# Kernel tuning notes

Measured on AMD Instinct MI355X. Metric: run time of the kernel, lower is better.

Reference implementation:

```python
import jax, jax.numpy as jnp
import numpy as np

B, N, D, L = 8, 2048, 1024, 128


def setup_inputs() -> dict:
    key = jax.random.key(0)
    ks = jax.random.split(key, 8)
    return {
        "e_i_t_minus_1": jax.random.normal(ks[0], (B, D), dtype=jnp.float32),
        "e_j_t": jax.random.normal(ks[1], (B, N, D), dtype=jnp.float32),
        "imp_j_t": jax.random.uniform(ks[2], (B, N), dtype=jnp.float32),
        "R_lk": jax.random.normal(ks[3], (L, D), dtype=jnp.float32),
        "W_q": jax.random.normal(ks[4], (D, D), dtype=jnp.float32) * (D ** -0.5),
        "W_k": jax.random.normal(ks[5], (D, D), dtype=jnp.float32) * (D ** -0.5),
        "W_v": jax.random.normal(ks[6], (D, D), dtype=jnp.float32) * (D ** -0.5),
        "omega": jax.random.normal(ks[7], (D,), dtype=jnp.float32),
    }


def reference(e_i_t_minus_1, e_j_t, imp_j_t, R_lk, W_q, W_k, W_v, omega):
    # torch nn.Linear(x) = x @ W.T  (weights stored [out, in])
    q_i = jnp.einsum('bd,ed->be', e_i_t_minus_1, W_q)[:, None, :]   # [B,1,D]
    k_j = jnp.einsum('bnd,ed->bne', e_j_t, W_k)                      # [B,N,D]
    sigma = jnp.einsum('bnd,d->bn', jnp.tanh(q_i + k_j), omega)      # [B,N]
    exp_sigma = jnp.exp(sigma)
    sum_exp = jnp.sum(exp_sigma, axis=1, keepdims=True)              # [B,1]
    a_ij = imp_j_t * exp_sigma / (sum_exp + 1e-9)                    # [B,N]
    v_j = jnp.einsum('bnd,ed->bne', e_j_t, W_v)                      # [B,N,D]
    A = jnp.einsum('bn,bnd->bd', a_ij, v_j)                          # [B,D]
    # R_lk[l,d] * a_ij[b,n] * v_j[b,n,d], summed over n -> [B,L,D]
    A_lk = jnp.einsum('bn,bnd,ld->bld', a_ij, v_j, R_lk)             # [B,L,D]
    A_l = A                                                          # identical math in source
    return (A, A_lk, A_l)
```

## Files before the change

### kernel.cpp

```cpp
#include <hip/hip_runtime.h>
#include <hip/hip_bf16.h>
#include <math.h>

#define BB 8
#define NN 2048
#define DD 1024
#define LL 128
#define MM (BB*NN)

typedef _Float16 half8 __attribute__((ext_vector_type(8)));
typedef _Float16 half4 __attribute__((ext_vector_type(4)));
typedef __attribute__((ext_vector_type(4))) float floatx4;

__device__ __forceinline__ void glds16(const void* g, void* l) {
    __builtin_amdgcn_global_load_lds(
        (const __attribute__((address_space(1))) unsigned int*)g,
        (__attribute__((address_space(3))) unsigned int*)l, 16, 0, 0);
}

__device__ __forceinline__ float ftanh(float x) {
    float e = __expf(2.0f * x);
    return 1.0f - 2.0f * __builtin_amdgcn_rcpf(e + 1.0f);
}

__global__ __launch_bounds__(256) void prep_kernel(const float* __restrict__ e_j,
                                                   _Float16* __restrict__ eh,
                                                   const float* __restrict__ Wk,
                                                   _Float16* __restrict__ wh,
                                                   const float* __restrict__ e_i,
                                                   const float* __restrict__ Wq,
                                                   float* __restrict__ q) {
    __shared__ float us[BB][DD];
    int blk = blockIdx.x;
    int tid = threadIdx.x;
    if (blk < 8192) {
        int i = blk * 256 + tid;
        const float4* xp = (const float4*)e_j + (size_t)i * 2;
        float4 v0 = xp[0], v1 = xp[1];
        half8 h;
        h[0] = (_Float16)v0.x; h[1] = (_Float16)v0.y;
        h[2] = (_Float16)v0.z; h[3] = (_Float16)v0.w;
        h[4] = (_Float16)v1.x; h[5] = (_Float16)v1.y;
        h[6] = (_Float16)v1.z; h[7] = (_Float16)v1.w;
        *(half8*)(eh + (size_t)i * 8) = h;
    } else if (blk < 8704) {
        int i = (blk - 8192) * 256 + tid;
        const float4* xp = (const float4*)Wk + (size_t)i * 2;
        float4 v0 = xp[0], v1 = xp[1];
        half8 h;
        h[0] = (_Float16)v0.x; h[1] = (_Float16)v0.y;
        h[2] = (_Float16)v0.z; h[3] = (_Float16)v0.w;
        h[4] = (_Float16)v1.x; h[5] = (_Float16)v1.y;
        h[6] = (_Float16)v1.z; h[7] = (_Float16)v1.w;
        *(half8*)(wh + (size_t)i * 8) = h;
    } else {
        for (int i = tid; i < BB * DD / 4; i += 256)
            ((float4*)&us[0][0])[i] = ((const float4*)e_i)[i];
        __syncthreads();
        int w = tid >> 6, lane = tid & 63;
        int d = (blk - 8704) * 4 + w;
        float acc[8] = {0.f, 0.f, 0.f, 0.f, 0.f, 0.f, 0.f, 0.f};
        for (int e0 = 0; e0 < DD; e0 += 256) {
            float4 wv = *(const float4*)&Wq[(size_t)d * DD + e0 + lane * 4];
            #pragma unroll
            for (int r = 0; r < 8; ++r) {
                float4 uv = *(const float4*)&us[r][e0 + lane * 4];
                acc[r] += wv.x * uv.x + wv.y * uv.y + wv.z * uv.z + wv.w * uv.w;
            }
        }
        #pragma unroll
        for (int r = 0; r < 8; ++r) {
            float s = acc[r];
            #pragma unroll
            for (int off = 32; off; off >>= 1) s += __shfl_down(s, off, 64);
            if (lane == 0) q[r * DD + d] = s;
        }
    }
}

__global__ __launch_bounds__(512, 2) void sigma256(const _Float16* __restrict__ eh,
                                                   const _Float16* __restrict__ wh,
                                                   const float* __restrict__ q,
                                                   const float* __restrict__ omega,
                                                   float* __restrict__ sig_part)
{
    __shared__ _Float16 As[4][256][32];
    __shared__ _Float16 Bs[4][256][32];

    const int tid  = threadIdx.x;
    const int lane = tid & 63;
    const int wid  = tid >> 6;
    const int wr   = wid >> 2;
    const int wc   = wid & 3;
    const int c15  = lane & 15, quad = lane >> 4;

    const int wgid   = (blockIdx.x & 7) * 32 + (blockIdx.x >> 3);
    const int colBlk = wgid >> 6;
    const int rowBlk = wgid & 63;
    const int row0   = rowBlk * 256;
    const int col0   = colBlk * 256;
    const int b      = row0 / NN;

    const int srow = wid * 16 + (lane >> 2);
    const int ssub = ((lane & 3) ^ ((lane >> 3) & 3)) * 8;
    const _Float16* gA = eh + (size_t)(row0 + srow) * DD + ssub;
    const _Float16* gB = wh + (size_t)(col0 + srow) * DD + ssub;
    char* const ldsA0 = (char*)&As[0][0][0] + wid * 1024;
    char* const ldsB0 = (char*)&Bs[0][0][0] + wid * 1024;

#define STAGE_A(kt) do { int _bi = (kt) & 3; int _k0 = (kt) * 32;                  \
        glds16(gA + _k0,                    ldsA0 + _bi * 16384);                  \
        glds16(gA + (size_t)128 * DD + _k0, ldsA0 + _bi * 16384 + 8192); } while (0)
#define STAGE_B(kt) do { int _bi = (kt) & 3; int _k0 = (kt) * 32;                  \
        glds16(gB + _k0,                    ldsB0 + _bi * 16384);                  \
        glds16(gB + (size_t)128 * DD + _k0, ldsB0 + _bi * 16384 + 8192); } while (0)

    const char* const Abase = (const char*)&As[0][0][0];
    const char* const Bbase = (const char*)&Bs[0][0][0];
#define FRAG(base, bi, row, qd) \
    (*(const half8*)((base) + (bi) * 16384 + (row) * 64 + ((((qd) ^ (((row) >> 1) & 3))) << 4)))

    floatx4 acc[8][4];
    #pragma unroll
    for (int m = 0; m < 8; ++m)
        #pragma unroll
        for (int n = 0; n < 4; ++n) acc[m][n] = (floatx4){0.f, 0.f, 0.f, 0.f};

    half8 a03[4], a47[4], bb[4], bbn[4];

    STAGE_A(0); STAGE_B(0);
    STAGE_A(1); STAGE_B(1);
    STAGE_A(2); STAGE_B(2);
    asm volatile("s_waitcnt vmcnt(8)" ::: "memory");
    __builtin_amdgcn_s_barrier();
    __builtin_amdgcn_sched_barrier(0);
    #pragma unroll
    for (int n = 0; n < 4; ++n) bb[n]  = FRAG(Bbase, 0, wc * 64  + n * 16 + c15, quad);
    #pragma unroll
    for (int m = 0; m < 4; ++m) a03[m] = FRAG(Abase, 0, wr * 128 + m * 16 + c15, quad);

#define PH1(t_, DO_STAGE)                                                          \
    {                                                                              \
        const int bi = (t_) & 3;                                                   \
        _Pragma("unroll")                                                          \
        for (int m = 0; m < 4; ++m)                                                \
            a47[m] = FRAG(Abase, bi, wr * 128 + 64 + m * 16 + c15, quad);          \
        if (DO_STAGE) STAGE_A((t_) + 3);                                           \
        __builtin_amdgcn_sched_barrier(0);                                         \
        __builtin_amdgcn_s_setprio(1);                                             \
        _Pragma("unroll")                                                          \
        for (int m = 0; m < 4; ++m)                                                \
            _Pragma("unroll")                                                      \
            for (int n = 0; n < 4; ++n)                                            \
                acc[m][n] = __builtin_amdgcn_mfma_f32_16x16x32_f16(a03[m], bb[n], acc[m][n], 0, 0, 0); \
        __builtin_amdgcn_s_setprio(0);                                             \
    }

#define PH2(t_, DO_STAGE, DO_READS, VMW)                                           \
    {                                                                              \
        const int bin = ((t_) + 1) & 3;                                            \
        asm volatile("s_waitcnt vmcnt(" #VMW ")" ::: "memory");                    \
        asm volatile("s_waitcnt lgkmcnt(0)" ::: "memory");                         \
        __builtin_amdgcn_s_barrier();                                              \
        __builtin_amdgcn_sched_barrier(0);                                         \
        if (DO_READS) {                                                            \
            _Pragma("unroll")                                                      \
            for (int n = 0; n < 4; ++n)                                            \
                bbn[n] = FRAG(Bbase, bin, wc * 64  + n * 16 + c15, quad);          \
            _Pragma("unroll")                                                      \
            for (int m = 0; m < 4; ++m)                                            \
                a03[m] = FRAG(Abase, bin, wr * 128 + m * 16 + c15, quad);          \
        }                                                                          \
        if (DO_STAGE) STAGE_B((t_) + 3);                                           \
        __builtin_amdgcn_sched_barrier(0);                                         \
        __builtin_amdgcn_s_setprio(1);                                             \
        _Pragma("unroll")                                                          \
        for (int m = 0; m < 4; ++m)                                                \
            _Pragma("unroll")                                                      \
            for (int n = 0; n < 4; ++n)                                            \
                acc[4 + m][n] = __builtin_amdgcn_mfma_f32_16x16x32_f16(a47[m], bb[n], acc[4 + m][n], 0, 0, 0); \
        __builtin_amdgcn_s_setprio(0);                                             \
        if (DO_READS) {                                                            \
            _Pragma("unroll")                                                      \
            for (int n = 0; n < 4; ++n) bb[n] = bbn[n];                            \
        }                                                                          \
    }

    for (int tt = 0; tt < 28; tt += 4) {
        PH1(tt + 0, 1) PH2(tt + 0, 1, 1, 6)
        PH1(tt + 1, 1) PH2(tt + 1, 1, 1, 6)
        PH1(tt + 2, 1) PH2(tt + 2, 1, 1, 6)
        PH1(tt + 3, 1) PH2(tt + 3, 1, 1, 6)
    }
    PH1(28, 1) PH2(28, 1, 1, 6)
    PH1(29, 0) PH2(29, 0, 1, 4)
    PH1(30, 0) PH2(30, 0, 1, 0)
    PH1(31, 0) PH2(31, 0, 0, 0)

#undef PH1
#undef PH2
#undef FRAG
#undef STAGE_A
#undef STAGE_B

    float part[8][4];
    #pragma unroll
    for (int m = 0; m < 8; ++m)
        #pragma unroll
        for (int r = 0; r < 4; ++r) part[m][r] = 0.f;

    #pragma unroll
    for (int n = 0; n < 4; ++n) {
        int col = col0 + wc * 64 + n * 16 + c15;
        float qv = q[b * DD + col];
        float om = omega[col];
        #pragma unroll
        for (int m = 0; m < 8; ++m)
            #pragma unroll
            for (int r = 0; r < 4; ++r)
                part[m][r] += ftanh(acc[m][n][r] + qv) * om;
    }

    float (*red)[4] = (float(*)[4])&As[0][0][0];
    #pragma unroll
    for (int m = 0; m < 8; ++m)
        #pragma unroll
        for (int r = 0; r < 4; ++r) {
            float s = part[m][r];
            s += __shfl_xor(s, 1, 64);
            s += __shfl_xor(s, 2, 64);
            s += __shfl_xor(s, 4, 64);
            s += __shfl_xor(s, 8, 64);
            if (c15 == 0) red[wr * 128 + m * 16 + quad * 4 + r][wc] = s;
        }
    __syncthreads();
    if (tid < 256)
        sig_part[(size_t)colBlk * MM + row0 + tid] =
            red[tid][0] + red[tid][1] + red[tid][2] + red[tid][3];
}

__global__ __launch_bounds__(256) void softmax_k(const float* __restrict__ sig_part,
                                                 const float* __restrict__ imp,
                                                 float* __restrict__ a_ij) {
    int b = blockIdx.x >> 3, slice = blockIdx.x & 7;
    int tid = threadIdx.x;
    __shared__ float red[256];
    float sv[8];
    float m = -1e30f;
    #pragma unroll
    for (int p = 0; p < 8; ++p) {
        int n = p * 256 + tid;
        float s = 0.f;
        #pragma unroll
        for (int db = 0; db < 4; ++db) s += sig_part[db * MM + b * NN + n];
        sv[p] = s;
        m = fmaxf(m, s);
    }
    red[tid] = m; __syncthreads();
    for (int off = 128; off; off >>= 1) {
        if (tid < off) red[tid] = fmaxf(red[tid], red[tid + off]);
        __syncthreads();
    }
    m = red[0]; __syncthreads();
    float sum = 0.f;
    #pragma unroll
    for (int p = 0; p < 8; ++p) sum += expf(sv[p] - m);
    red[tid] = sum; __syncthreads();
    for (int off = 128; off; off >>= 1) {
        if (tid < off) red[tid] += red[tid + off];
        __syncthreads();
    }
    float inv = 1.f / (red[0] + 1e-9f * expf(-m));
    int n = slice * 256 + tid;
    a_ij[b * NN + n] = imp[b * NN + n] * expf(sv[slice] - m) * inv;
}

__global__ __launch_bounds__(256) void u_kernel(const float* __restrict__ a_ij,
                                                const _Float16* __restrict__ eh,
                                                float* __restrict__ u_part) {
    int b = blockIdx.x >> 7, nc = blockIdx.x & 127;
    int t = threadIdx.x;
    float4 acc = {0.f, 0.f, 0.f, 0.f};
    const _Float16* base = eh + ((size_t)(b * NN + nc * 16)) * DD + t * 4;
    const float* ap = a_ij + b * NN + nc * 16;
    #pragma unroll
    for (int n = 0; n < 16; ++n) {
        float a = ap[n];
        half4 v = *(const half4*)(base + (size_t)n * DD);
        acc.x += a * (float)v[0]; acc.y += a * (float)v[1];
        acc.z += a * (float)v[2]; acc.w += a * (float)v[3];
    }
    *(float4*)(u_part + ((size_t)nc * BB + b) * DD + t * 4) = acc;
}

__global__ __launch_bounds__(256) void ureduce(const float* __restrict__ u_part,
                                               float* __restrict__ u) {
    int i = blockIdx.x * 256 + threadIdx.x;
    float s = 0.f;
    #pragma unroll 8
    for (int nc = 0; nc < 128; ++nc) s += u_part[(size_t)nc * BB * DD + i];
    u[i] = s;
}

__global__ __launch_bounds__(256) void rowdot8(const float* __restrict__ X,
                                               const float* __restrict__ W,
                                               float* __restrict__ out) {
    __shared__ float us[BB][DD];
    int tid = threadIdx.x;
    for (int i = tid; i < BB * DD / 4; i += 256)
        ((float4*)&us[0][0])[i] = ((const float4*)X)[i];
    __syncthreads();
    int w = tid >> 6, lane = tid & 63;
    int d = blockIdx.x * 4 + w;
    float acc[8] = {0.f, 0.f, 0.f, 0.f, 0.f, 0.f, 0.f, 0.f};
    for (int e0 = 0; e0 < DD; e0 += 256) {
        float4 wv = *(const float4*)&W[(size_t)d * DD + e0 + lane * 4];
        #pragma unroll
        for (int r = 0; r < 8; ++r) {
            float4 uv = *(const float4*)&us[r][e0 + lane * 4];
            acc[r] += wv.x * uv.x + wv.y * uv.y + wv.z * uv.z + wv.w * uv.w;
        }
    }
    #pragma unroll
    for (int r = 0; r < 8; ++r) {
        float s = acc[r];
        #pragma unroll
        for (int off = 32; off; off >>= 1) s += __shfl_down(s, off, 64);
        if (lane == 0) out[r * DD + d] = s;
    }
}

__global__ __launch_bounds__(256) void out_kernel(const float* __restrict__ A,
                                                  const float* __restrict__ Rlk,
                                                  float* __restrict__ out) {
    int i = blockIdx.x * 256 + threadIdx.x;
    int d = i & (DD - 1);
    int l = (i >> 10) & (LL - 1);
    int b = i >> 17;
    out[BB * DD + i] = A[b * DD + d] * Rlk[l * DD + d];
    if (i < BB * DD) {
        out[i] = A[i];
        out[BB * DD + BB * LL * DD + i] = A[i];
    }
}

extern "C" void kernel_launch(void* const* d_in, const int* in_sizes, int n_in,
                              void* d_out, int out_size, void* d_ws, size_t ws_size,
                              hipStream_t stream) {
    const float* e_i   = (const float*)d_in[0];
    const float* e_j   = (const float*)d_in[1];
    const float* imp   = (const float*)d_in[2];
    const float* Rlk   = (const float*)d_in[3];
    const float* Wq    = (const float*)d_in[4];
    const float* Wk    = (const float*)d_in[5];
    const float* Wv    = (const float*)d_in[6];
    const float* omega = (const float*)d_in[7];
    float* out = (float*)d_out;
    float* ws  = (float*)d_ws;

    float* q    = ws;
    float* sigp = ws + 8192;
    float* a_ij = ws + 139264;
    float* u    = ws + 155648;
    _Float16* eh = (_Float16*)(ws + 172032);
    _Float16* wh = eh + (size_t)MM * DD;
    float* u_part = (float*)(wh + (size_t)DD * DD);

    prep_kernel<<<8960, 256, 0, stream>>>(e_j, eh, Wk, wh, e_i, Wq, q);

    sigma256<<<dim3(256), 512, 0, stream>>>(eh, wh, q, omega, sigp);

    softmax_k<<<64, 256, 0, stream>>>(sigp, imp, a_ij);

    u_kernel<<<1024, 256, 0, stream>>>(a_ij, eh, u_part);
    ureduce<<<32, 256, 0, stream>>>(u_part, u);

    rowdot8<<<256, 256, 0, stream>>>(u, Wv, a_ij);

    out_kernel<<<(BB * LL * DD) / 256, 256, 0, stream>>>(a_ij, Rlk, out);
}
```

Before: 191.4 us.

## Shrink sigma GEMM tile to 128x256 with 4 waves and triple buffering

Replaces the 256x256-tile, 8-wave sigma GEMM with a 128x256 tile run by 4 waves, launching 512 workgroups instead of 256. The LDS ring drops from four stages to three, and the split two-phase MFMA schedule becomes one tile-per-step loop in which each wave holds all 8 A fragments. The aim is to fill all CUs (256 blocks underfill a 256-CU MI355X at two blocks per CU) and to simplify pipelining. The cost is lower arithmetic intensity per tile, since each B tile is reloaded for twice as many row blocks, plus higher register use per wave.

```diff
diff --git a/kernel.cpp b/kernel.cpp
--- a/kernel.cpp
+++ b/kernel.cpp
@@ -78,26 +78,25 @@
     }
 }
 
-__global__ __launch_bounds__(512, 2) void sigma256(const _Float16* __restrict__ eh,
+__global__ __launch_bounds__(256, 2) void sigma128(const _Float16* __restrict__ eh,
                                                    const _Float16* __restrict__ wh,
                                                    const float* __restrict__ q,
                                                    const float* __restrict__ omega,
                                                    float* __restrict__ sig_part)
 {
-    __shared__ _Float16 As[4][256][32];
-    __shared__ _Float16 Bs[4][256][32];
+    __shared__ _Float16 As[3][128][32];
+    __shared__ _Float16 Bs[3][256][32];
 
     const int tid  = threadIdx.x;
     const int lane = tid & 63;
     const int wid  = tid >> 6;
-    const int wr   = wid >> 2;
-    const int wc   = wid & 3;
+    const int wc   = wid;
     const int c15  = lane & 15, quad = lane >> 4;
 
-    const int wgid   = (blockIdx.x & 7) * 32 + (blockIdx.x >> 3);
-    const int colBlk = wgid >> 6;
-    const int rowBlk = wgid & 63;
-    const int row0   = rowBlk * 256;
+    const int wgid   = (blockIdx.x & 7) * 64 + (blockIdx.x >> 3);
+    const int colBlk = wgid >> 7;
+    const int rowBlk = wgid & 127;
+    const int row0   = rowBlk * 128;
     const int col0   = colBlk * 256;
     const int b      = row0 / NN;
 
@@ -108,17 +107,20 @@
     char* const ldsA0 = (char*)&As[0][0][0] + wid * 1024;
     char* const ldsB0 = (char*)&Bs[0][0][0] + wid * 1024;
 
-#define STAGE_A(kt) do { int _bi = (kt) & 3; int _k0 = (kt) * 32;                  \
-        glds16(gA + _k0,                    ldsA0 + _bi * 16384);                  \
-        glds16(gA + (size_t)128 * DD + _k0, ldsA0 + _bi * 16384 + 8192); } while (0)
-#define STAGE_B(kt) do { int _bi = (kt) & 3; int _k0 = (kt) * 32;                  \
-        glds16(gB + _k0,                    ldsB0 + _bi * 16384);                  \
-        glds16(gB + (size_t)128 * DD + _k0, ldsB0 + _bi * 16384 + 8192); } while (0)
+#define STAGE(kt, bi_) do { const int _k0 = (kt) * 32;                             \
+        glds16(gA + _k0,                    ldsA0 + (bi_) * 8192);                 \
+        glds16(gA + (size_t)64  * DD + _k0, ldsA0 + (bi_) * 8192  + 4096);         \
+        glds16(gB + _k0,                    ldsB0 + (bi_) * 16384);                \
+        glds16(gB + (size_t)64  * DD + _k0, ldsB0 + (bi_) * 16384 + 4096);         \
+        glds16(gB + (size_t)128 * DD + _k0, ldsB0 + (bi_) * 16384 + 8192);         \
+        glds16(gB + (size_t)192 * DD + _k0, ldsB0 + (bi_) * 16384 + 12288); } while (0)
 
     const char* const Abase = (const char*)&As[0][0][0];
     const char* const Bbase = (const char*)&Bs[0][0][0];
-#define FRAG(base, bi, row, qd) \
-    (*(const half8*)((base) + (bi) * 16384 + (row) * 64 + ((((qd) ^ (((row) >> 1) & 3))) << 4)))
+#define FRAGA(bi, row, qd) \
+    (*(const half8*)(Abase + (bi) * 8192  + (row) * 64 + ((((qd) ^ (((row) >> 1) & 3))) << 4)))
+#define FRAGB(bi, row, qd) \
+    (*(const half8*)(Bbase + (bi) * 16384 + (row) * 64 + ((((qd) ^ (((row) >> 1) & 3))) << 4)))
 
     floatx4 acc[8][4];
     #pragma unroll
@@ -126,82 +128,42 @@
         #pragma unroll
         for (int n = 0; n < 4; ++n) acc[m][n] = (floatx4){0.f, 0.f, 0.f, 0.f};
 
-    half8 a03[4], a47[4], bb[4], bbn[4];
-
-    STAGE_A(0); STAGE_B(0);
-    STAGE_A(1); STAGE_B(1);
-    STAGE_A(2); STAGE_B(2);
-    asm volatile("s_waitcnt vmcnt(8)" ::: "memory");
-    __builtin_amdgcn_s_barrier();
-    __builtin_amdgcn_sched_barrier(0);
-    #pragma unroll
-    for (int n = 0; n < 4; ++n) bb[n]  = FRAG(Bbase, 0, wc * 64  + n * 16 + c15, quad);
-    #pragma unroll
-    for (int m = 0; m < 4; ++m) a03[m] = FRAG(Abase, 0, wr * 128 + m * 16 + c15, quad);
-
-#define PH1(t_, DO_STAGE)                                                          \
+    STAGE(0, 0);
+    STAGE(1, 1);
+
+#define TILE(t_, bi_, DO_STAGE, VMW)                                               \
     {                                                                              \
-        const int bi = (t_) & 3;                                                   \
+        asm volatile("s_waitcnt vmcnt(" #VMW ")" ::: "memory");                    \
+        __builtin_amdgcn_s_barrier();                                              \
+        __builtin_amdgcn_sched_barrier(0);                                         \
+        half8 a[8], bv[4];                                                         \
         _Pragma("unroll")                                                          \
-        for (int m = 0; m < 4; ++m)                                                \
-            a47[m] = FRAG(Abase, bi, wr * 128 + 64 + m * 16 + c15, quad);          \
-        if (DO_STAGE) STAGE_A((t_) + 3);                                           \
+        for (int n = 0; n < 4; ++n) bv[n] = FRAGB(bi_, wc * 64 + n * 16 + c15, quad); \
+        _Pragma("unroll")                                                          \
+        for (int m = 0; m < 8; ++m) a[m]  = FRAGA(bi_, m * 16 + c15, quad);        \
+        if (DO_STAGE) STAGE((t_) + 2, ((t_) + 2) % 3);                             \
         __builtin_amdgcn_sched_barrier(0);                                         \
         __builtin_amdgcn_s_setprio(1);                                             \
         _Pragma("unroll")                                                          \
-        for (int m = 0; m < 4; ++m)                                                \
+        for (int m = 0; m < 8; ++m)                                                \
             _Pragma("unroll")                                                      \
             for (int n = 0; n < 4; ++n)                                            \
-                acc[m][n] = __builtin_amdgcn_mfma_f32_16x16x32_f16(a03[m], bb[n], acc[m][n], 0, 0, 0); \
+                acc[m][n] = __builtin_amdgcn_mfma_f32_16x16x32_f16(a[m], bv[n], acc[m][n], 0, 0, 0); \
         __builtin_amdgcn_s_setprio(0);                                             \
     }
 
-#define PH2(t_, DO_STAGE, DO_READS, VMW)                                           \
-    {                                                                              \
-        const int bin = ((t_) + 1) & 3;                                            \
-        asm volatile("s_waitcnt vmcnt(" #VMW ")" ::: "memory");                    \
-        asm volatile("s_waitcnt lgkmcnt(0)" ::: "memory");                         \
-        __builtin_amdgcn_s_barrier();                                              \
-        __builtin_amdgcn_sched_barrier(0);                                         \
-        if (DO_READS) {                                                            \
-            _Pragma("unroll")                                                      \
-            for (int n = 0; n < 4; ++n)                                            \
-                bbn[n] = FRAG(Bbase, bin, wc * 64  + n * 16 + c15, quad);          \
-            _Pragma("unroll")                                                      \
-            for (int m = 0; m < 4; ++m)                                            \
-                a03[m] = FRAG(Abase, bin, wr * 128 + m * 16 + c15, quad);          \
-        }                                                                          \
-        if (DO_STAGE) STAGE_B((t_) + 3);                                           \
-        __builtin_amdgcn_sched_barrier(0);                                         \
-        __builtin_amdgcn_s_setprio(1);                                             \
-        _Pragma("unroll")                                                          \
-        for (int m = 0; m < 4; ++m)                                                \
-            _Pragma("unroll")                                                      \
-            for (int n = 0; n < 4; ++n)                                            \
-                acc[4 + m][n] = __builtin_amdgcn_mfma_f32_16x16x32_f16(a47[m], bb[n], acc[4 + m][n], 0, 0, 0); \
-        __builtin_amdgcn_s_setprio(0);                                             \
-        if (DO_READS) {                                                            \
-            _Pragma("unroll")                                                      \
-            for (int n = 0; n < 4; ++n) bb[n] = bbn[n];                            \
-        }                                                                          \
-    }
-
-    for (int tt = 0; tt < 28; tt += 4) {
-        PH1(tt + 0, 1) PH2(tt + 0, 1, 1, 6)
-        PH1(tt + 1, 1) PH2(tt + 1, 1, 1, 6)
-        PH1(tt + 2, 1) PH2(tt + 2, 1, 1, 6)
-        PH1(tt + 3, 1) PH2(tt + 3, 1, 1, 6)
-    }
-    PH1(28, 1) PH2(28, 1, 1, 6)
-    PH1(29, 0) PH2(29, 0, 1, 4)
-    PH1(30, 0) PH2(30, 0, 1, 0)
-    PH1(31, 0) PH2(31, 0, 0, 0)
-
-#undef PH1
-#undef PH2
-#undef FRAG
-#undef STAGE_A
-#undef STAGE_B
+    for (int tt = 0; tt < 30; tt += 3) {
+        TILE(tt + 0, 0, 1, 6)
+        TILE(tt + 1, 1, 1, 6)
+        TILE(tt + 2, 2, 1, 6)
+    }
+    TILE(30, 0, 0, 6)
+    TILE(31, 1, 0, 0)
+
+#undef TILE
+#undef FRAGA
+#undef FRAGB
+#undef STAGE
 
     float part[8][4];
     #pragma unroll
@@ -231,10 +193,10 @@
             s += __shfl_xor(s, 2, 64);
             s += __shfl_xor(s, 4, 64);
             s += __shfl_xor(s, 8, 64);
-            if (c15 == 0) red[wr * 128 + m * 16 + quad * 4 + r][wc] = s;
+            if (c15 == 0) red[m * 16 + quad * 4 + r][wc] = s;
         }
     __syncthreads();
-    if (tid < 256)
+    if (tid < 128)
         sig_part[(size_t)colBlk * MM + row0 + tid] =
             red[tid][0] + red[tid][1] + red[tid][2] + red[tid][3];
 }
@@ -368,7 +330,7 @@
 
     prep_kernel<<<8960, 256, 0, stream>>>(e_j, eh, Wk, wh, e_i, Wq, q);
 
-    sigma256<<<dim3(256), 512, 0, stream>>>(eh, wh, q, omega, sigp);
+    sigma128<<<dim3(512), 256, 0, stream>>>(eh, wh, q, omega, sigp);
 
     softmax_k<<<64, 256, 0, stream>>>(sigp, imp, a_ij);
 
```

New measurement: 191.9 us. About the same (+0.3%).
